# Performance work log

Hardware: AMD Instinct MI355X
Metric: run time of the kernel (lower is better)

Reference implementation:

```python
import jax, jax.numpy as jnp
import numpy as np

F = 26
D = 128
B = 16384
# upper-triangular (offset=1) index pairs over (F+1)x(F+1)
_TRIU_I, _TRIU_J = np.triu_indices(F + 1, k=1)
_TRIU_I = jnp.asarray(_TRIU_I)
_TRIU_J = jnp.asarray(_TRIU_J)


def setup_inputs() -> dict:
    key = jax.random.key(0)
    k1, k2 = jax.random.split(key)
    sparse_x = jax.random.normal(k1, (B, F, D), dtype=jnp.float32)
    dense_x = jax.random.normal(k2, (B, D), dtype=jnp.float32)
    return {"sparse_x": sparse_x, "dense_x": dense_x}


def reference(sparse_x, dense_x):
    # combined: [B, F+1, D] -- dense feature appended as one extra row
    combined = jnp.concatenate([sparse_x, dense_x[:, None, :]], axis=1)
    # pairwise dot products: [B, F+1, F+1]
    interact = jnp.einsum('bfd,bgd->bfg', combined, combined)
    # gather strict upper triangle -> [B, K] where K = (F+1)*F/2
    return interact[:, _TRIU_I, _TRIU_J]
```

## Files before the change

kernel.cpp:

```cpp
#include <hip/hip_runtime.h>


constexpr int kRows  = 27;
constexpr int kD     = 128;
constexpr int kPitch = 132;
constexpr int kPairs = 351;

__global__ void interact_fp32_kernel(
    const float* __restrict__ sparse_x,
    const float* __restrict__ dense_x,
    float* __restrict__ out)
{
    __shared__ float X[kRows * kPitch];
    const int t = threadIdx.x;
    const int b = blockIdx.x;

    for (int e = t; e < 864; e += 384) {
        const int f   = e * 4;
        const int row = f >> 7;
        const int col = f & 127;
        float4 v;
        if (row < 26) {
            v = *reinterpret_cast<const float4*>(sparse_x + (size_t)b * (26 * kD) + f);
        } else {
            v = *reinterpret_cast<const float4*>(dense_x + (size_t)b * kD + col);
        }
        *reinterpret_cast<float4*>(&X[row * kPitch + col]) = v;
    }
    __syncthreads();

    if (t < kPairs) {
        int p = t, i = 0;
        while (p >= (26 - i)) { p -= (26 - i); ++i; }
        const int j = i + 1 + p;

        const float* ri = &X[i * kPitch];
        const float* rj = &X[j * kPitch];
        float acc = 0.f;
        #pragma unroll
        for (int d4 = 0; d4 < kD / 4; ++d4) {
            float4 a = *reinterpret_cast<const float4*>(ri + d4 * 4);
            float4 c = *reinterpret_cast<const float4*>(rj + d4 * 4);
            acc += a.x * c.x + a.y * c.y + a.z * c.z + a.w * c.w;
        }
        out[(size_t)b * kPairs + t] = acc;
    }
}

extern "C" void kernel_launch(void* const* d_in, const int* in_sizes, int n_in,
                              void* d_out, int out_size, void* d_ws, size_t ws_size,
                              hipStream_t stream) {
    const float* sparse_x = (const float*)d_in[0];
    const float* dense_x  = (const float*)d_in[1];
    float* out = (float*)d_out;
    const int B = in_sizes[1] / kD;
    interact_fp32_kernel<<<B, 384, 0, stream>>>(sparse_x, dense_x, out);
}
```

Baseline: 305.2 us.

## Compute pairwise interactions with bf16 MFMA, four batches per block

Replaces the per-thread fp32 dot-product loop with bf16 MFMA 16x16x32 instructions. Inputs are converted to bf16 while staged into padded LDS, and each wave computes the 27x27 Gram matrix of one batch element as three 16x16 tiles. Four batch elements share a 256-thread block, and the pad rows are zeroed. This cuts ALU and LDS-read work, but fp32 inputs are rounded to bf16, which lowers accuracy and may break the tolerance. The kernel stays largely bound by memory traffic.

```diff
diff --git a/kernel.cpp b/kernel.cpp
--- a/kernel.cpp
+++ b/kernel.cpp
@@ -1,49 +1,99 @@
 #include <hip/hip_runtime.h>
 
+constexpr int kRows   = 27;
+constexpr int kD      = 128;
+constexpr int kKP     = 136;
+constexpr int kSlot   = 32 * kKP;
+constexpr int kNB     = 4;
+constexpr int kPairs  = 351;
 
-constexpr int kRows  = 27;
-constexpr int kD     = 128;
-constexpr int kPitch = 132;
-constexpr int kPairs = 351;
+typedef __attribute__((ext_vector_type(8))) short bf16x8;
+typedef __attribute__((ext_vector_type(4))) float f32x4;
 
-__global__ void interact_fp32_kernel(
+__device__ __forceinline__ unsigned short to_bf16(float f) {
+    union { float f; unsigned u; } x; x.f = f;
+    unsigned u = x.u;
+    return (unsigned short)((u + 0x7fffu + ((u >> 16) & 1u)) >> 16);
+}
+
+__device__ __forceinline__ int triu_idx(int i, int j) {
+    return (i * (53 - i)) / 2 + (j - i - 1);
+}
+
+__global__ __launch_bounds__(256) void interact_kernel(
     const float* __restrict__ sparse_x,
     const float* __restrict__ dense_x,
     float* __restrict__ out)
 {
-    __shared__ float X[kRows * kPitch];
-    const int t = threadIdx.x;
-    const int b = blockIdx.x;
+    __shared__ short lds[kNB * kSlot];
+    const int t  = threadIdx.x;
+    const int b0 = blockIdx.x * kNB;
 
-    for (int e = t; e < 864; e += 384) {
-        const int f   = e * 4;
-        const int row = f >> 7;
-        const int col = f & 127;
-        float4 v;
-        if (row < 26) {
-            v = *reinterpret_cast<const float4*>(sparse_x + (size_t)b * (26 * kD) + f);
-        } else {
-            v = *reinterpret_cast<const float4*>(dense_x + (size_t)b * kD + col);
+    {
+        const ushort4 z = {0, 0, 0, 0};
+        #pragma unroll
+        for (int e = t; e < 640; e += 256) {
+            const int slot = e / 160;
+            const int rem  = e - slot * 160;
+            const int row  = 27 + (rem >> 5);
+            const int c4   = (rem & 31) * 4;
+            *reinterpret_cast<ushort4*>(&lds[slot * kSlot + row * kKP + c4]) = z;
         }
-        *reinterpret_cast<float4*>(&X[row * kPitch + col]) = v;
+    }
+
+    const float4* sp = reinterpret_cast<const float4*>(sparse_x + (size_t)b0 * (26 * kD));
+    #pragma unroll
+    for (int it = 0; it < 13; ++it) {
+        const int e = t + it * 256;
+        float4 v = sp[e];
+        const int f    = e * 4;
+        const int slot = f / 3328;
+        const int rem  = f - slot * 3328;
+        const int row  = rem >> 7;
+        const int col  = rem & 127;
+        ushort4 h;
+        h.x = to_bf16(v.x); h.y = to_bf16(v.y);
+        h.z = to_bf16(v.z); h.w = to_bf16(v.w);
+        *reinterpret_cast<ushort4*>(&lds[slot * kSlot + row * kKP + col]) = h;
+    }
+    if (t < 32 * kNB) {
+        const int slot = t >> 5;
+        const int c4   = (t & 31) * 4;
+        float4 v = *reinterpret_cast<const float4*>(dense_x + (size_t)(b0 + slot) * kD + c4);
+        ushort4 h;
+        h.x = to_bf16(v.x); h.y = to_bf16(v.y);
+        h.z = to_bf16(v.z); h.w = to_bf16(v.w);
+        *reinterpret_cast<ushort4*>(&lds[slot * kSlot + 26 * kKP + c4]) = h;
     }
     __syncthreads();
 
-    if (t < kPairs) {
-        int p = t, i = 0;
-        while (p >= (26 - i)) { p -= (26 - i); ++i; }
-        const int j = i + 1 + p;
+    const int wave = t >> 6;
+    const int lane = t & 63;
+    const short* X = &lds[wave * kSlot];
+    const int m    = lane & 15;
+    const int quad = lane >> 4;
 
-        const float* ri = &X[i * kPitch];
-        const float* rj = &X[j * kPitch];
-        float acc = 0.f;
-        #pragma unroll
-        for (int d4 = 0; d4 < kD / 4; ++d4) {
-            float4 a = *reinterpret_cast<const float4*>(ri + d4 * 4);
-            float4 c = *reinterpret_cast<const float4*>(rj + d4 * 4);
-            acc += a.x * c.x + a.y * c.y + a.z * c.z + a.w * c.w;
-        }
-        out[(size_t)b * kPairs + t] = acc;
+    f32x4 c00 = {0.f, 0.f, 0.f, 0.f};
+    f32x4 c01 = {0.f, 0.f, 0.f, 0.f};
+    f32x4 c11 = {0.f, 0.f, 0.f, 0.f};
+
+    #pragma unroll
+    for (int k0 = 0; k0 < kD; k0 += 32) {
+        bf16x8 a0 = *reinterpret_cast<const bf16x8*>(&X[m * kKP + quad * 8 + k0]);
+        bf16x8 a1 = *reinterpret_cast<const bf16x8*>(&X[(16 + m) * kKP + quad * 8 + k0]);
+        c00 = __builtin_amdgcn_mfma_f32_16x16x32_bf16(a0, a0, c00, 0, 0, 0);
+        c01 = __builtin_amdgcn_mfma_f32_16x16x32_bf16(a0, a1, c01, 0, 0, 0);
+        c11 = __builtin_amdgcn_mfma_f32_16x16x32_bf16(a1, a1, c11, 0, 0, 0);
+    }
+
+    float* ob = out + (size_t)(b0 + wave) * kPairs;
+    const int j = m;
+    #pragma unroll
+    for (int r = 0; r < 4; ++r) {
+        const int i = quad * 4 + r;
+        if (i < j)                        ob[triu_idx(i, j)]           = c00[r];
+        if (16 + j < kRows)               ob[triu_idx(i, 16 + j)]      = c01[r];
+        if (i < j && 16 + j < kRows)      ob[triu_idx(16 + i, 16 + j)] = c11[r];
     }
 }
 
@@ -54,5 +104,5 @@
     const float* dense_x  = (const float*)d_in[1];
     float* out = (float*)d_out;
     const int B = in_sizes[1] / kD;
-    interact_fp32_kernel<<<B, 384, 0, stream>>>(sparse_x, dense_x, out);
+    interact_kernel<<<B / kNB, 256, 0, stream>>>(sparse_x, dense_x, out);
 }
```

Measured after the change: 306.0 us (median of 2 runs). About the same (+0.3%).
